# Kernel tuning notes

Measured on AMD Instinct MI355X. Metric: run time of the kernel, lower is better.

Reference implementation:

```python
import jax, jax.numpy as jnp
import numpy as np

B, N1, N2, DIM = 16, 1024, 4096, 512
EPS_BN = 1e-5   # torch BatchNorm1d default eps
EPS_FP = 1e-8   # PointNet++ FP inverse-distance eps


def setup_inputs() -> dict:
    key = jax.random.key(0)
    ks = jax.random.split(key, 6)
    s1 = 1.0 / np.sqrt(2 * DIM)
    s2 = 1.0 / np.sqrt(DIM)
    return {
        "xyz1": jax.random.normal(ks[0], (B, N1, 3), jnp.float32),
        "points1": jax.random.normal(ks[1], (B, N1, 2 * DIM), jnp.float32),
        "xyz2": jax.random.normal(ks[2], (B, N2, 3), jnp.float32),
        "points2": jax.random.normal(ks[3], (B, N2, DIM), jnp.float32),
        "fc1_w": jax.random.normal(ks[4], (2 * DIM, DIM), jnp.float32) * s1,
        "fc1_b": jnp.zeros((DIM,), jnp.float32),
        "bn1_gamma": jnp.ones((DIM,), jnp.float32),
        "bn1_beta": jnp.zeros((DIM,), jnp.float32),
        "fc2_w": jax.random.normal(ks[5], (DIM, DIM), jnp.float32) * s2,
        "fc2_b": jnp.zeros((DIM,), jnp.float32),
        "bn2_gamma": jnp.ones((DIM,), jnp.float32),
        "bn2_beta": jnp.zeros((DIM,), jnp.float32),
    }


def _bn_relu(x, gamma, beta):
    # BatchNorm1d (training mode, batch stats) over (B, L) per channel; x is [B, L, C]
    mu = jnp.mean(x, axis=(0, 1), keepdims=True)
    var = jnp.var(x, axis=(0, 1), keepdims=True)
    return jax.nn.relu((x - mu) * jax.lax.rsqrt(var + EPS_BN) * gamma + beta)


def _fp_interpolate(xyz_dst, xyz_src, feats_src):
    # PointNet++ inverse-distance 3-NN interpolation.
    # xyz_dst [B,N,3], xyz_src [B,S,3], feats_src [B,S,C] -> [B,N,C]
    d = (jnp.sum(xyz_dst * xyz_dst, -1)[:, :, None]
         + jnp.sum(xyz_src * xyz_src, -1)[:, None, :]
         - 2.0 * jnp.einsum('bnd,bsd->bns', xyz_dst, xyz_src))  # squared dists [B,N,S]
    neg_d3, idx3 = jax.lax.top_k(-d, 3)                          # 3 smallest dists
    w = 1.0 / (-neg_d3 + EPS_FP)                                  # [B,N,3]
    w = w / jnp.sum(w, -1, keepdims=True)
    # gather: [B,1,S,C] indexed along axis 2 by [B,N,3,1] -> [B,N,3,C]
    gathered = jnp.take_along_axis(feats_src[:, None, :, :], idx3[..., None], axis=2)
    return jnp.einsum('bnkc,bnk->bnc', gathered, w)


def reference(xyz1, points1, xyz2, points2,
              fc1_w, fc1_b, bn1_gamma, bn1_beta,
              fc2_w, fc2_b, bn2_gamma, bn2_beta):
    feats1 = _bn_relu(points1 @ fc1_w + fc1_b, bn1_gamma, bn1_beta)   # [B,N1,DIM]
    feats1 = _fp_interpolate(xyz2, xyz1, feats1)                      # [B,N2,DIM]
    feats2 = _bn_relu(points2 @ fc2_w + fc2_b, bn2_gamma, bn2_beta)   # [B,N2,DIM]
    return (xyz2, feats1 + feats2)
```

## Files before the change

### kernel.cpp

```cpp
#include <hip/hip_runtime.h>
#include <stdint.h>

typedef unsigned short u16;
typedef __attribute__((ext_vector_type(8))) short short8;
typedef __attribute__((ext_vector_type(4))) float floatx4;

#define BB 16
#define NN1 1024
#define NN2 4096
#define DIM 512
#define M1 (BB*NN1)
#define M2 (BB*NN2)

__device__ __forceinline__ float bf2f(u16 u){
  union { unsigned int i; float f; } v; v.i = ((unsigned int)u) << 16; return v.f;
}
__device__ __forceinline__ u16 f2bf(float f){
  union { float f; unsigned int i; } v; v.f = f;
  unsigned int i = v.i;
  return (u16)((i + 0x7FFFu + ((i >> 16) & 1u)) >> 16);
}

__device__ __forceinline__ uint32_t cvtpk(float lo, float hi){
  uint32_t r;
  asm("v_cvt_pk_bf16_f32 %0, %1, %2" : "=v"(r) : "v"(lo), "v"(hi));
  return r;
}

__device__ __forceinline__ void gload_lds16(const void* g, void* l){
  __builtin_amdgcn_global_load_lds(
      (const __attribute__((address_space(1))) void*)g,
      (__attribute__((address_space(3))) void*)l, 16, 0, 0);
}

__global__ void prep(const float* __restrict__ fc1_w, const float* __restrict__ fc2_w,
                     u16* __restrict__ wT1, u16* __restrict__ wT2,
                     float* __restrict__ stats){
  int idx = blockIdx.x * 256 + threadIdx.x;
  if (idx < 2048) stats[idx] = 0.0f;
  if (idx < 512 * 1024){
    int n = idx >> 10, k = idx & 1023;
    wT1[idx] = f2bf(fc1_w[k * 512 + n]);
  } else {
    int j = idx - 512 * 1024;
    int n = j >> 9, k = j & 511;
    wT2[j] = f2bf(fc2_w[k * 512 + n]);
  }
}

__global__ __launch_bounds__(256) void gemm_mfma(
    const float* __restrict__ A, const u16* __restrict__ BT,
    const float* __restrict__ bias, void* __restrict__ Yv,
    int M, int K, int out_is_f32,
    float* __restrict__ sum, float* __restrict__ sumsq)
{
  const int N = 512;
  __shared__ u16 As[128 * 32];
  __shared__ u16 Bs[128 * 32];
  int tid  = threadIdx.x;
  int lane = tid & 63, wave = tid >> 6;

  int id = blockIdx.x;
  int bm = (id & 7) + ((id >> 5) << 3);
  int bn = (id >> 3) & 3;

  int wm = (wave & 1) * 64, wn = (wave >> 1) * 64;
  int r16 = lane & 15, quad = lane >> 4;

  floatx4 acc[4][4];
  for (int i = 0; i < 4; i++)
    for (int j = 0; j < 4; j++)
      acc[i][j] = (floatx4)(0.0f);

  int lr = tid >> 2;
  int kc = tid & 3;

  const float* Ag = A  + (size_t)(bm * 128) * K;
  const u16*   Bg = BT + (size_t)(bn * 128) * K;

  int pb0 = wave * 128 + lane;
  int rb0 = pb0 >> 2, cb0 = (pb0 & 3) ^ ((rb0 >> 1) & 3);
  int pb1 = pb0 + 64;
  int rb1 = pb1 >> 2, cb1 = (pb1 & 3) ^ ((rb1 >> 1) & 3);
  const u16* bsrc0 = Bg + (size_t)rb0 * K + cb0 * 8;
  const u16* bsrc1 = Bg + (size_t)rb1 * K + cb1 * 8;
  u16* bdst0 = &Bs[(wave * 128) * 8];
  u16* bdst1 = &Bs[(wave * 128 + 64) * 8];

  int rsw = ((r16 >> 1) & 3) ^ quad;

  for (int k0 = 0; k0 < K; k0 += 32){
    gload_lds16(bsrc0 + k0, bdst0);
    gload_lds16(bsrc1 + k0, bdst1);
    for (int rr = 0; rr < 2; rr++){
      int row = lr + rr * 64;
      const float* ap = Ag + (size_t)row * K + k0 + kc * 8;
      float4 a0 = *(const float4*)ap;
      float4 a1 = *(const float4*)(ap + 4);
      uint4 tv;
      tv.x = cvtpk(a0.x, a0.y);
      tv.y = cvtpk(a0.z, a0.w);
      tv.z = cvtpk(a1.x, a1.y);
      tv.w = cvtpk(a1.z, a1.w);
      int dst = row * 32 + ((kc ^ ((row >> 1) & 3)) * 8);
      *(uint4*)(&As[dst]) = tv;
    }
    __syncthreads();
    short8 af[4], bfr[4];
    for (int i = 0; i < 4; i++) af[i]  = *(const short8*)(&As[(wm + i*16 + r16) * 32 + rsw * 8]);
    for (int j = 0; j < 4; j++) bfr[j] = *(const short8*)(&Bs[(wn + j*16 + r16) * 32 + rsw * 8]);
    for (int i = 0; i < 4; i++)
      for (int j = 0; j < 4; j++)
        acc[i][j] = __builtin_amdgcn_mfma_f32_16x16x32_bf16(af[i], bfr[j], acc[i][j], 0, 0, 0);
    __syncthreads();
  }

  float cs[4] = {0.f, 0.f, 0.f, 0.f};
  float cq[4] = {0.f, 0.f, 0.f, 0.f};
  for (int i = 0; i < 4; i++){
    int rowb = bm * 128 + wm + i * 16 + quad * 4;
    for (int j = 0; j < 4; j++){
      int col = bn * 128 + wn + j * 16 + r16;
      float bv = bias[col];
      for (int r = 0; r < 4; r++){
        float v = acc[i][j][r] + bv;
        cs[j] += v; cq[j] += v * v;
        size_t idx = (size_t)(rowb + r) * N + col;
        if (out_is_f32) ((float*)Yv)[idx] = v;
        else            ((u16*)Yv)[idx]   = f2bf(v);
      }
    }
  }

  for (int j = 0; j < 4; j++){
    cs[j] += __shfl_xor(cs[j], 16); cs[j] += __shfl_xor(cs[j], 32);
    cq[j] += __shfl_xor(cq[j], 16); cq[j] += __shfl_xor(cq[j], 32);
  }
  float* S = (float*)As;
  if (lane < 16){
    int wmh = wave & 1, wnh = wave >> 1;
    for (int j = 0; j < 4; j++){
      int c = wnh * 64 + j * 16 + r16;
      S[wmh * 256 + c]       = cs[j];
      S[wmh * 256 + 128 + c] = cq[j];
    }
  }
  __syncthreads();
  {
    int stat = tid >> 7, c = tid & 127;
    float v = S[stat * 128 + c] + S[256 + stat * 128 + c];
    float* dstp = stat ? sumsq : sum;
    atomicAdd(&dstp[bn * 128 + c], v);
  }
}

__global__ void bn_coeff_copy(const float* __restrict__ stats,
                              const float* __restrict__ g1, const float* __restrict__ be1,
                              const float* __restrict__ g2, const float* __restrict__ be2,
                              float* __restrict__ coef,
                              const uint4* __restrict__ xsrc, uint4* __restrict__ xdst){
  int b = blockIdx.x, tid = threadIdx.x;
  if (b == 0){
    int c = tid;
    {
      float mu  = stats[c] / (float)M1;
      float var = stats[512 + c] / (float)M1 - mu * mu;
      var = fmaxf(var, 0.0f);
      float a = g1[c] * (1.0f / sqrtf(var + 1e-5f));
      coef[c] = a;
      coef[512 + c] = be1[c] - mu * a;
    }
    {
      float mu  = stats[1024 + c] / (float)M2;
      float var = stats[1536 + c] / (float)M2 - mu * mu;
      var = fmaxf(var, 0.0f);
      float a = g2[c] * (1.0f / sqrtf(var + 1e-5f));
      coef[1024 + c] = a;
      coef[1536 + c] = be2[c] - mu * a;
    }
  } else {
    int i = (b - 1) * 512 + tid;
    xdst[i] = xsrc[i];
  }
}

__global__ __launch_bounds__(64) void interp_final(
    const float* __restrict__ xyz1, const float* __restrict__ xyz2,
    const u16* __restrict__ Y1, const float* __restrict__ coef,
    float* __restrict__ outF)
{
  int lane = threadIdx.x;
  int bid  = blockIdx.x;
  int b = bid >> 12;

  const float* pd = xyz2 + (size_t)bid * 3;
  double xd = (double)pd[0];
  double yd = (double)pd[1];
  double zd = (double)pd[2];

  double dl[16];
  const float* ps = xyz1 + (size_t)b * NN1 * 3;
  for (int s = 0; s < 16; s++){
    const float* q = ps + (s * 64 + lane) * 3;
    double dx = xd - (double)q[0];
    double dy = yd - (double)q[1];
    double dz = zd - (double)q[2];
    dl[s] = dx * dx + dy * dy + dz * dz;
  }

  double dsel[3]; int isel[3];
  for (int p = 0; p < 3; p++){
    double dm = dl[0]; int sm = 0;
    for (int s = 1; s < 16; s++) if (dl[s] < dm){ dm = dl[s]; sm = s; }
    int im = sm * 64 + lane;
    for (int off = 1; off < 64; off <<= 1){
      double od = __shfl_xor(dm, off);
      int    oi = __shfl_xor(im, off);
      if (od < dm || (od == dm && oi < im)){ dm = od; im = oi; }
    }
    dsel[p] = dm; isel[p] = im;
    if ((im & 63) == lane) dl[im >> 6] = 1e300;
  }

  double w0 = 1.0 / (dsel[0] + 1e-8);
  double w1 = 1.0 / (dsel[1] + 1e-8);
  double w2 = 1.0 / (dsel[2] + 1e-8);
  double wsum = w0 + w1 + w2;
  float f0 = (float)(w0 / wsum), f1 = (float)(w1 / wsum), f2 = (float)(w2 / wsum);

  const u16* r0 = Y1 + (size_t)(b * NN1 + isel[0]) * DIM;
  const u16* r1 = Y1 + (size_t)(b * NN1 + isel[1]) * DIM;
  const u16* r2 = Y1 + (size_t)(b * NN1 + isel[2]) * DIM;
  float* o = outF + (size_t)bid * DIM;

  int c0 = lane * 8;
  uint4 q0 = *(const uint4*)(r0 + c0);
  uint4 q1 = *(const uint4*)(r1 + c0);
  uint4 q2 = *(const uint4*)(r2 + c0);
  float4 ylo = *(const float4*)(o + c0);
  float4 yhi = *(const float4*)(o + c0 + 4);
  const u16* p0 = (const u16*)&q0;
  const u16* p1 = (const u16*)&q1;
  const u16* p2 = (const u16*)&q2;
  float yv[8] = { ylo.x, ylo.y, ylo.z, ylo.w, yhi.x, yhi.y, yhi.z, yhi.w };
  float res[8];
  for (int j = 0; j < 8; j++){
    int c = c0 + j;
    float a1 = coef[c],        b1 = coef[512 + c];
    float a2 = coef[1024 + c], b2 = coef[1536 + c];
    float v0 = fmaxf(a1 * bf2f(p0[j]) + b1, 0.0f);
    float v1 = fmaxf(a1 * bf2f(p1[j]) + b1, 0.0f);
    float v2 = fmaxf(a1 * bf2f(p2[j]) + b1, 0.0f);
    float vi = f0 * v0 + f1 * v1 + f2 * v2;
    float y2 = fmaxf(a2 * yv[j] + b2, 0.0f);
    res[j] = vi + y2;
  }
  *(float4*)(o + c0)     = make_float4(res[0], res[1], res[2], res[3]);
  *(float4*)(o + c0 + 4) = make_float4(res[4], res[5], res[6], res[7]);
}

extern "C" void kernel_launch(void* const* d_in, const int* in_sizes, int n_in,
                              void* d_out, int out_size, void* d_ws, size_t ws_size,
                              hipStream_t stream){
  const float* xyz1    = (const float*)d_in[0];
  const float* points1 = (const float*)d_in[1];
  const float* xyz2    = (const float*)d_in[2];
  const float* points2 = (const float*)d_in[3];
  const float* fc1_w   = (const float*)d_in[4];
  const float* fc1_b   = (const float*)d_in[5];
  const float* bn1_g   = (const float*)d_in[6];
  const float* bn1_b   = (const float*)d_in[7];
  const float* fc2_w   = (const float*)d_in[8];
  const float* fc2_b   = (const float*)d_in[9];
  const float* bn2_g   = (const float*)d_in[10];
  const float* bn2_b   = (const float*)d_in[11];

  char* ws = (char*)d_ws;
  u16*   Y1    = (u16*)(ws);
  u16*   wT1   = (u16*)(ws + 16777216);
  u16*   wT2   = (u16*)(ws + 17825792);
  float* stats = (float*)(ws + 18350080);
  float* coef  = (float*)(ws + 18358272);

  float* out  = (float*)d_out;
  float* outF = out + 196608;

  prep<<<3072, 256, 0, stream>>>(fc1_w, fc2_w, wT1, wT2, stats);

  gemm_mfma<<<512, 256, 0, stream>>>(points1, wT1, fc1_b, Y1,   M1, 1024, 0,
                                     stats,        stats + 512);
  gemm_mfma<<<2048, 256, 0, stream>>>(points2, wT2, fc2_b, outF, M2,  512, 1,
                                      stats + 1024, stats + 1536);

  bn_coeff_copy<<<97, 512, 0, stream>>>(stats, bn1_g, bn1_b, bn2_g, bn2_b, coef,
                                        (const uint4*)xyz2, (uint4*)out);

  interp_final<<<65536, 64, 0, stream>>>(xyz1, xyz2, Y1, coef, outF);
}
```

Baseline: 465.0 us.

## Double-buffer GEMM tiles and pack distance/index keys in interpolation

The GEMM now double-buffers its LDS tiles: it loads the next K-slice of A (converted to bf16) and B while running MFMAs on the current slice, which roughly halves the barriers per step. The interpolation kernel packs each squared distance and its index into one 64-bit key by clearing the low 10 mantissa bits, so each top-3 pass is a single integer min-reduction across the wave. Inverse-distance weights move from double division to float hardware reciprocals, and the BN coefficients are read with vector loads. The trade-off is slightly lower precision, both in the truncated distances (which can change tie-breaks between near-equal distances) and in the approximate reciprocals.

```diff
diff --git a/kernel.cpp b/kernel.cpp
--- a/kernel.cpp
+++ b/kernel.cpp
@@ -25,6 +25,10 @@
   uint32_t r;
   asm("v_cvt_pk_bf16_f32 %0, %1, %2" : "=v"(r) : "v"(lo), "v"(hi));
   return r;
+}
+
+__device__ __forceinline__ float rcpf(float x){
+  float r; asm("v_rcp_f32 %0, %1" : "=v"(r) : "v"(x)); return r;
 }
 
 __device__ __forceinline__ void gload_lds16(const void* g, void* l){
@@ -55,8 +59,8 @@
     float* __restrict__ sum, float* __restrict__ sumsq)
 {
   const int N = 512;
-  __shared__ u16 As[128 * 32];
-  __shared__ u16 Bs[128 * 32];
+  __shared__ u16 As[2][128 * 32];
+  __shared__ u16 Bs[2][128 * 32];
   int tid  = threadIdx.x;
   int lane = tid & 63, wave = tid >> 6;
 
@@ -68,7 +72,9 @@
   int r16 = lane & 15, quad = lane >> 4;
 
   floatx4 acc[4][4];
+#pragma unroll
   for (int i = 0; i < 4; i++)
+#pragma unroll
     for (int j = 0; j < 4; j++)
       acc[i][j] = (floatx4)(0.0f);
 
@@ -77,6 +83,11 @@
 
   const float* Ag = A  + (size_t)(bm * 128) * K;
   const u16*   Bg = BT + (size_t)(bn * 128) * K;
+
+  const float* ap0 = Ag + (size_t)lr * K + kc * 8;
+  const float* ap1 = Ag + (size_t)(lr + 64) * K + kc * 8;
+  int adst0 = lr * 32 + ((kc ^ ((lr >> 1) & 3)) * 8);
+  int adst1 = adst0 + 64 * 32;
 
   int pb0 = wave * 128 + lane;
   int rb0 = pb0 >> 2, cb0 = (pb0 & 3) ^ ((rb0 >> 1) & 3);
@@ -84,44 +95,70 @@
   int rb1 = pb1 >> 2, cb1 = (pb1 & 3) ^ ((rb1 >> 1) & 3);
   const u16* bsrc0 = Bg + (size_t)rb0 * K + cb0 * 8;
   const u16* bsrc1 = Bg + (size_t)rb1 * K + cb1 * 8;
-  u16* bdst0 = &Bs[(wave * 128) * 8];
-  u16* bdst1 = &Bs[(wave * 128 + 64) * 8];
+  int boff = (wave * 128) * 8;
 
   int rsw = ((r16 >> 1) & 3) ^ quad;
 
-  for (int k0 = 0; k0 < K; k0 += 32){
-    gload_lds16(bsrc0 + k0, bdst0);
-    gload_lds16(bsrc1 + k0, bdst1);
-    for (int rr = 0; rr < 2; rr++){
-      int row = lr + rr * 64;
-      const float* ap = Ag + (size_t)row * K + k0 + kc * 8;
-      float4 a0 = *(const float4*)ap;
-      float4 a1 = *(const float4*)(ap + 4);
-      uint4 tv;
-      tv.x = cvtpk(a0.x, a0.y);
-      tv.y = cvtpk(a0.z, a0.w);
-      tv.z = cvtpk(a1.x, a1.y);
-      tv.w = cvtpk(a1.z, a1.w);
-      int dst = row * 32 + ((kc ^ ((row >> 1) & 3)) * 8);
-      *(uint4*)(&As[dst]) = tv;
-    }
-    __syncthreads();
+  int NS = K >> 5;
+  float4 a00, a01, a10, a11;
+
+  a00 = *(const float4*)(ap0);     a01 = *(const float4*)(ap0 + 4);
+  a10 = *(const float4*)(ap1);     a11 = *(const float4*)(ap1 + 4);
+  gload_lds16(bsrc0, &Bs[0][boff]);
+  gload_lds16(bsrc1, &Bs[0][boff + 512]);
+  {
+    uint4 tv0, tv1;
+    tv0.x = cvtpk(a00.x, a00.y); tv0.y = cvtpk(a00.z, a00.w);
+    tv0.z = cvtpk(a01.x, a01.y); tv0.w = cvtpk(a01.z, a01.w);
+    tv1.x = cvtpk(a10.x, a10.y); tv1.y = cvtpk(a10.z, a10.w);
+    tv1.z = cvtpk(a11.x, a11.y); tv1.w = cvtpk(a11.z, a11.w);
+    *(uint4*)(&As[0][adst0]) = tv0;
+    *(uint4*)(&As[0][adst1]) = tv1;
+  }
+  __syncthreads();
+
+  int cur = 0;
+  for (int ks = 0; ks < NS; ks++){
+    int k1 = (ks + 1) << 5;
+    if (ks + 1 < NS){
+      a00 = *(const float4*)(ap0 + k1); a01 = *(const float4*)(ap0 + k1 + 4);
+      a10 = *(const float4*)(ap1 + k1); a11 = *(const float4*)(ap1 + k1 + 4);
+      gload_lds16(bsrc0 + k1, &Bs[cur ^ 1][boff]);
+      gload_lds16(bsrc1 + k1, &Bs[cur ^ 1][boff + 512]);
+    }
     short8 af[4], bfr[4];
-    for (int i = 0; i < 4; i++) af[i]  = *(const short8*)(&As[(wm + i*16 + r16) * 32 + rsw * 8]);
-    for (int j = 0; j < 4; j++) bfr[j] = *(const short8*)(&Bs[(wn + j*16 + r16) * 32 + rsw * 8]);
+#pragma unroll
+    for (int i = 0; i < 4; i++) af[i]  = *(const short8*)(&As[cur][(wm + i*16 + r16) * 32 + rsw * 8]);
+#pragma unroll
+    for (int j = 0; j < 4; j++) bfr[j] = *(const short8*)(&Bs[cur][(wn + j*16 + r16) * 32 + rsw * 8]);
+#pragma unroll
     for (int i = 0; i < 4; i++)
+#pragma unroll
       for (int j = 0; j < 4; j++)
         acc[i][j] = __builtin_amdgcn_mfma_f32_16x16x32_bf16(af[i], bfr[j], acc[i][j], 0, 0, 0);
+    if (ks + 1 < NS){
+      uint4 tv0, tv1;
+      tv0.x = cvtpk(a00.x, a00.y); tv0.y = cvtpk(a00.z, a00.w);
+      tv0.z = cvtpk(a01.x, a01.y); tv0.w = cvtpk(a01.z, a01.w);
+      tv1.x = cvtpk(a10.x, a10.y); tv1.y = cvtpk(a10.z, a10.w);
+      tv1.z = cvtpk(a11.x, a11.y); tv1.w = cvtpk(a11.z, a11.w);
+      *(uint4*)(&As[cur ^ 1][adst0]) = tv0;
+      *(uint4*)(&As[cur ^ 1][adst1]) = tv1;
+    }
     __syncthreads();
+    cur ^= 1;
   }
 
   float cs[4] = {0.f, 0.f, 0.f, 0.f};
   float cq[4] = {0.f, 0.f, 0.f, 0.f};
+#pragma unroll
   for (int i = 0; i < 4; i++){
     int rowb = bm * 128 + wm + i * 16 + quad * 4;
+#pragma unroll
     for (int j = 0; j < 4; j++){
       int col = bn * 128 + wn + j * 16 + r16;
       float bv = bias[col];
+#pragma unroll
       for (int r = 0; r < 4; r++){
         float v = acc[i][j][r] + bv;
         cs[j] += v; cq[j] += v * v;
@@ -132,6 +169,7 @@
     }
   }
 
+#pragma unroll
   for (int j = 0; j < 4; j++){
     cs[j] += __shfl_xor(cs[j], 16); cs[j] += __shfl_xor(cs[j], 32);
     cq[j] += __shfl_xor(cq[j], 16); cq[j] += __shfl_xor(cq[j], 32);
@@ -139,6 +177,7 @@
   float* S = (float*)As;
   if (lane < 16){
     int wmh = wave & 1, wnh = wave >> 1;
+#pragma unroll
     for (int j = 0; j < 4; j++){
       int c = wnh * 64 + j * 16 + r16;
       S[wmh * 256 + c]       = cs[j];
@@ -198,39 +237,50 @@
   double yd = (double)pd[1];
   double zd = (double)pd[2];
 
-  double dl[16];
+  unsigned long long kl[16];
   const float* ps = xyz1 + (size_t)b * NN1 * 3;
+#pragma unroll
   for (int s = 0; s < 16; s++){
     const float* q = ps + (s * 64 + lane) * 3;
     double dx = xd - (double)q[0];
     double dy = yd - (double)q[1];
     double dz = zd - (double)q[2];
-    dl[s] = dx * dx + dy * dy + dz * dz;
-  }
-
-  double dsel[3]; int isel[3];
+    double d = dx * dx + dy * dy + dz * dz;
+    unsigned long long bits = (unsigned long long)__double_as_longlong(d);
+    kl[s] = (bits & ~1023ULL) | (unsigned long long)(s * 64 + lane);
+  }
+
+  unsigned long long selk[3];
   for (int p = 0; p < 3; p++){
-    double dm = dl[0]; int sm = 0;
-    for (int s = 1; s < 16; s++) if (dl[s] < dm){ dm = dl[s]; sm = s; }
-    int im = sm * 64 + lane;
+    unsigned long long m = kl[0];
+#pragma unroll
+    for (int s = 1; s < 16; s++) if (kl[s] < m) m = kl[s];
     for (int off = 1; off < 64; off <<= 1){
-      double od = __shfl_xor(dm, off);
-      int    oi = __shfl_xor(im, off);
-      if (od < dm || (od == dm && oi < im)){ dm = od; im = oi; }
-    }
-    dsel[p] = dm; isel[p] = im;
-    if ((im & 63) == lane) dl[im >> 6] = 1e300;
-  }
-
-  double w0 = 1.0 / (dsel[0] + 1e-8);
-  double w1 = 1.0 / (dsel[1] + 1e-8);
-  double w2 = 1.0 / (dsel[2] + 1e-8);
-  double wsum = w0 + w1 + w2;
-  float f0 = (float)(w0 / wsum), f1 = (float)(w1 / wsum), f2 = (float)(w2 / wsum);
-
-  const u16* r0 = Y1 + (size_t)(b * NN1 + isel[0]) * DIM;
-  const u16* r1 = Y1 + (size_t)(b * NN1 + isel[1]) * DIM;
-  const u16* r2 = Y1 + (size_t)(b * NN1 + isel[2]) * DIM;
+      unsigned long long o = (unsigned long long)__shfl_xor((long long)m, off);
+      if (o < m) m = o;
+    }
+    selk[p] = m;
+    if (p < 2){
+#pragma unroll
+      for (int s = 0; s < 16; s++) if (kl[s] == m) kl[s] = ~0ULL;
+    }
+  }
+
+  int i0 = (int)(selk[0] & 1023ULL);
+  int i1 = (int)(selk[1] & 1023ULL);
+  int i2 = (int)(selk[2] & 1023ULL);
+  float d0 = (float)__longlong_as_double((long long)(selk[0] & ~1023ULL));
+  float d1 = (float)__longlong_as_double((long long)(selk[1] & ~1023ULL));
+  float d2 = (float)__longlong_as_double((long long)(selk[2] & ~1023ULL));
+  float w0 = rcpf(d0 + 1e-8f);
+  float w1 = rcpf(d1 + 1e-8f);
+  float w2 = rcpf(d2 + 1e-8f);
+  float inv = rcpf(w0 + w1 + w2);
+  float f0 = w0 * inv, f1 = w1 * inv, f2 = w2 * inv;
+
+  const u16* r0 = Y1 + (size_t)(b * NN1 + i0) * DIM;
+  const u16* r1 = Y1 + (size_t)(b * NN1 + i1) * DIM;
+  const u16* r2 = Y1 + (size_t)(b * NN1 + i2) * DIM;
   float* o = outF + (size_t)bid * DIM;
 
   int c0 = lane * 8;
@@ -239,15 +289,20 @@
   uint4 q2 = *(const uint4*)(r2 + c0);
   float4 ylo = *(const float4*)(o + c0);
   float4 yhi = *(const float4*)(o + c0 + 4);
+  union { float4 v[2]; float f[8]; } A1u, B1u, A2u, B2u;
+  A1u.v[0] = *(const float4*)(coef + c0);        A1u.v[1] = *(const float4*)(coef + c0 + 4);
+  B1u.v[0] = *(const float4*)(coef + 512 + c0);  B1u.v[1] = *(const float4*)(coef + 512 + c0 + 4);
+  A2u.v[0] = *(const float4*)(coef + 1024 + c0); A2u.v[1] = *(const float4*)(coef + 1024 + c0 + 4);
+  B2u.v[0] = *(const float4*)(coef + 1536 + c0); B2u.v[1] = *(const float4*)(coef + 1536 + c0 + 4);
   const u16* p0 = (const u16*)&q0;
   const u16* p1 = (const u16*)&q1;
   const u16* p2 = (const u16*)&q2;
   float yv[8] = { ylo.x, ylo.y, ylo.z, ylo.w, yhi.x, yhi.y, yhi.z, yhi.w };
   float res[8];
+#pragma unroll
   for (int j = 0; j < 8; j++){
-    int c = c0 + j;
-    float a1 = coef[c],        b1 = coef[512 + c];
-    float a2 = coef[1024 + c], b2 = coef[1536 + c];
+    float a1 = A1u.f[j], b1 = B1u.f[j];
+    float a2 = A2u.f[j], b2 = B2u.f[j];
     float v0 = fmaxf(a1 * bf2f(p0[j]) + b1, 0.0f);
     float v1 = fmaxf(a1 * bf2f(p1[j]) + b1, 0.0f);
     float v2 = fmaxf(a1 * bf2f(p2[j]) + b1, 0.0f);
```

After: 462.1 us. Within noise of the previous version (-0.6%).
